# Performance work log

Measured on AMD Instinct MI355X. Metric: run time of the kernel, lower is better.

Reference implementation:

```python
import jax, jax.numpy as jnp
import numpy as np

D = 512  # common_dim

def _ln(x, g, b):
    m = jnp.mean(x, -1, keepdims=True)
    v = jnp.var(x, -1, keepdims=True)
    return g * (x - m) * jax.lax.rsqrt(v + 1e-5) + b

def _gelu(x):
    return jax.nn.gelu(x, approximate=False)  # torch nn.GELU default (erf)

def _mha(q, kv, Wi, bi, Wo, bo):
    # seq_len == 1: softmax over a single key is exactly 1 regardless of q/k,
    # so MultiheadAttention reduces to out_proj(v_proj(kv)); identical math,
    # and q/k projections receive exactly zero gradient either way.
    vp = kv @ Wi[:, 2 * D:] + bi[2 * D:]
    return vp @ Wo + bo

def setup_inputs() -> dict:
    key = jax.random.key(0)
    ks = iter(jax.random.split(key, 64))
    B, HID = 8192, 1024
    Fv, Fi, Ft = 10, 6, 15
    def rn(shape, s=0.02):
        return jax.random.normal(next(ks), shape, jnp.float32) * s
    return dict(
        verb_hidden=rn((B, HID), 1.0), verb_logits=rn((B, Fv), 1.0),
        inst_hidden=rn((B, HID), 1.0), inst_logits=rn((B, Fi), 1.0),
        target_hidden=rn((B, HID), 1.0), target_logits=rn((B, Ft), 1.0),
        # hidden_projection per task (order: verb, instrument, target)
        hp_W=rn((3, HID, D)), hp_b=jnp.zeros((3, D)), hp_g=jnp.ones((3, D)), hp_be=jnp.zeros((3, D)),
        # logit_projection per task (different in-dims)
        lp_W_verb=rn((Fv, D // 2)), lp_b_verb=jnp.zeros((D // 2,)),
        lp_W_inst=rn((Fi, D // 2)), lp_b_inst=jnp.zeros((D // 2,)),
        lp_W_target=rn((Ft, D // 2)), lp_b_target=jnp.zeros((D // 2,)),
        lp_g=jnp.ones((3, D // 2)), lp_be=jnp.zeros((3, D // 2)),
        # 4 MHA modules: [self, verb_inst, verb_target, inst_target]
        mha_in_W=rn((4, D, 3 * D)), mha_in_b=jnp.zeros((4, 3 * D)),
        mha_out_W=rn((4, D, D)), mha_out_b=jnp.zeros((4, D)),
        n1_g=jnp.ones((3, D)), n1_be=jnp.zeros((3, D)),
        n2_g=jnp.ones((3, D)), n2_be=jnp.zeros((3, D)),
        gate_W=rn((3, 2 * D, D)), gate_b=jnp.zeros((3, D)),
        fus_W1=rn((3 * D + 3 * (D // 2), D)), fus_b1=jnp.zeros((D,)),
        fus_g1=jnp.ones((D,)), fus_ge1=jnp.zeros((D,)),
        fus_W2=rn((D, D)), fus_b2=jnp.zeros((D,)),
        fus_g2=jnp.ones((D,)), fus_ge2=jnp.zeros((D,)),
    )

def reference(verb_hidden, verb_logits, inst_hidden, inst_logits, target_hidden, target_logits,
              hp_W, hp_b, hp_g, hp_be,
              lp_W_verb, lp_b_verb, lp_W_inst, lp_b_inst, lp_W_target, lp_b_target, lp_g, lp_be,
              mha_in_W, mha_in_b, mha_out_W, mha_out_b,
              n1_g, n1_be, n2_g, n2_be, gate_W, gate_b,
              fus_W1, fus_b1, fus_g1, fus_ge1, fus_W2, fus_b2, fus_g2, fus_ge2):
    # dropout is inference-mode identity
    def hproj(x, i):
        return _gelu(_ln(x @ hp_W[i] + hp_b[i], hp_g[i], hp_be[i]))
    def lproj(x, W, b, i):
        return _gelu(_ln(jax.nn.sigmoid(x) @ W + b, lp_g[i], lp_be[i]))

    verb_h, inst_h, target_h = hproj(verb_hidden, 0), hproj(inst_hidden, 1), hproj(target_hidden, 2)
    verb_l = lproj(verb_logits, lp_W_verb, lp_b_verb, 0)
    inst_l = lproj(inst_logits, lp_W_inst, lp_b_inst, 1)
    target_l = lproj(target_logits, lp_W_target, lp_b_target, 2)

    sa = lambda x: _mha(x, x, mha_in_W[0], mha_in_b[0], mha_out_W[0], mha_out_b[0])
    verb_e = _ln(verb_h + sa(verb_h), n1_g[0], n1_be[0])
    inst_e = _ln(inst_h + sa(inst_h), n1_g[1], n1_be[1])
    target_e = _ln(target_h + sa(target_h), n1_g[2], n1_be[2])

    ca = lambda i, q, kv: _mha(q, kv, mha_in_W[i], mha_in_b[i], mha_out_W[i], mha_out_b[i])
    v2i, i2v = ca(1, verb_e, inst_e), ca(1, inst_e, verb_e)
    v2t, t2v = ca(2, verb_e, target_e), ca(2, target_e, verb_e)
    i2t, t2i = ca(3, inst_e, target_e), ca(3, target_e, inst_e)

    def fuse(x, a, b, i):
        m = (a + b) * 0.5
        gate = jax.nn.sigmoid(jnp.concatenate([x, m], axis=1) @ gate_W[i] + gate_b[i])
        return _ln(x + gate * m, n2_g[i], n2_be[i])

    verb_f = fuse(verb_e, v2i, v2t, 0)
    inst_f = fuse(inst_e, i2v, i2t, 1)
    target_f = fuse(target_e, t2v, t2i, 2)

    comb = jnp.concatenate([verb_f, inst_f, target_f, verb_l, inst_l, target_l], axis=1)  # [B, 2304]
    h = _gelu(_ln(comb @ fus_W1 + fus_b1, fus_g1, fus_ge1))
    return _ln(h @ fus_W2 + fus_b2, fus_g2, fus_ge2)
```

## Files before the change

### kernel.cpp

```cpp
#include <hip/hip_runtime.h>
#include <math.h>

typedef unsigned short ushort_t;
using short8  = __attribute__((ext_vector_type(8))) short;
using floatx4 = __attribute__((ext_vector_type(4))) float;

__device__ __forceinline__ ushort_t f2bf(float f) {
  unsigned u = __builtin_bit_cast(unsigned, f);
  u = (u + 0x7fffu + ((u >> 16) & 1u)) >> 16;
  return (ushort_t)u;
}
__device__ __forceinline__ float bf2f(ushort_t u) {
  unsigned v = ((unsigned)u) << 16;
  return __builtin_bit_cast(float, v);
}

__device__ __forceinline__ void load_lds16(const ushort_t* g, ushort_t* l) {
  __builtin_amdgcn_global_load_lds(
      (const __attribute__((address_space(1))) unsigned int*)g,
      (__attribute__((address_space(3))) unsigned int*)l, 16, 0, 0);
}

struct Seg { const ushort_t* A; const ushort_t* W; int lda, ldw, K; };
struct GemmZ {
  ushort_t* Cb;
  ushort_t* CbT;
  const float* bias;
  float scale; int nseg; int mmax;
  Seg seg[6];
};
struct GemmArgs { GemmZ z[9]; };

template <int BM, int BK>
__device__ __forceinline__ void gemm_body(const GemmArgs& ga) {
  const GemmZ& gz = ga.z[blockIdx.z];
  if ((int)blockIdx.x >= gz.mmax) return;
  __shared__ ushort_t As[BM * BK];
  __shared__ ushort_t Bs[128 * BK];
  constexpr int TPR = BK / 8;
  constexpr int RPC = 2048 / BK;
  const int tid = threadIdx.x;
  const int wid = tid >> 6, lane = tid & 63, quad = lane >> 4, l16 = lane & 15;
  const int bm = blockIdx.x * BM, bn = blockIdx.y * 128;
  constexpr int MI = BM / 32;
  const int wm = (wid & 1) * (BM / 2), wn = (wid >> 1) * 64;
  floatx4 acc[MI][4] = {};
  const int srow = tid / TPR;
  const int scol = ((tid & (TPR - 1)) ^ (srow & (TPR - 1))) << 3;

  for (int s = 0; s < gz.nseg; s++) {
    const Seg sg = gz.seg[s];
    const ushort_t* aG = sg.A + (size_t)(bm + srow) * sg.lda + scol;
    const ushort_t* bG = sg.W + (size_t)(bn + srow) * sg.ldw + scol;
    for (int k0 = 0; k0 < sg.K; k0 += BK) {
      __syncthreads();
#pragma unroll
      for (int r = 0; r < BM / RPC; r++)
        load_lds16(aG + k0 + (size_t)(RPC * r) * sg.lda, As + r * 2048 + tid * 8);
#pragma unroll
      for (int r = 0; r < 128 / RPC; r++)
        load_lds16(bG + k0 + (size_t)(RPC * r) * sg.ldw, Bs + r * 2048 + tid * 8);
      __syncthreads();
#pragma unroll
      for (int sub = 0; sub < BK / 32; sub++) {
        const int sl = ((sub * 4 + quad) ^ (l16 & (TPR - 1))) << 3;
        short8 bw[4];
#pragma unroll
        for (int j = 0; j < 4; j++)
          bw[j] = *(const short8*)&Bs[(wn + 16 * j + l16) * BK + sl];
#pragma unroll
        for (int i = 0; i < MI; i++) {
          short8 af = *(const short8*)&As[(wm + 16 * i + l16) * BK + sl];
#pragma unroll
          for (int j = 0; j < 4; j++)
            acc[i][j] = __builtin_amdgcn_mfma_f32_16x16x32_bf16(af, bw[j], acc[i][j], 0, 0, 0);
        }
      }
    }
  }

#pragma unroll
  for (int i = 0; i < MI; i++) {
#pragma unroll
    for (int j = 0; j < 4; j++) {
      const int colg = bn + wn + 16 * j + l16;
      const float bb = gz.bias ? gz.bias[colg] : 0.f;
#pragma unroll
      for (int r = 0; r < 4; r++) {
        const int rowg = bm + wm + 16 * i + quad * 4 + r;
        const float v = (acc[i][j][r] + bb) * gz.scale;
        const ushort_t bo = f2bf(v);
        if (gz.Cb)  gz.Cb[(size_t)rowg * 512 + colg] = bo;
        if (gz.CbT) gz.CbT[(size_t)colg * 512 + rowg] = bo;
      }
    }
  }
}

__global__ __launch_bounds__(256) void gemm_L2(GemmArgs ga)  { gemm_body<128, 128>(ga); }
__global__ __launch_bounds__(256) void gemm_L4(GemmArgs ga)  { gemm_body<128, 128>(ga); }
__global__ __launch_bounds__(256) void gemm_L7(GemmArgs ga)  { gemm_body<128, 64>(ga); }
__global__ __launch_bounds__(256) void gemm_L9(GemmArgs ga)  { gemm_body<128, 64>(ga); }
__global__ __launch_bounds__(256) void gemm_L11(GemmArgs ga) { gemm_body<64, 128>(ga); }
__global__ __launch_bounds__(256) void gemm_L13(GemmArgs ga) { gemm_body<64, 128>(ga); }

__global__ __launch_bounds__(256) void row_ln(
    const ushort_t* __restrict__ P, const ushort_t* __restrict__ R,
    const ushort_t* __restrict__ cross,
    const float* __restrict__ gamma, const float* __restrict__ beta, int gstride,
    ushort_t* __restrict__ outb, float* __restrict__ outf, int mode, int gelu)
{
  const size_t S2 = (size_t)8192 * 512;
  const int wid = threadIdx.x >> 6, lane = threadIdx.x & 63;
  const int row = blockIdx.x * 4 + wid;
  const int t = row >> 13;
  const float* g  = gamma + t * gstride;
  const float* be = beta + t * gstride;
  const int c0 = lane * 8;
  const short8 pv = *(const short8*)&P[(size_t)row * 512 + c0];
  short8 rv = {}, av = {};
  if (mode >= 1) rv = *(const short8*)&R[(size_t)row * 512 + c0];
  if (mode == 2) av = *(const short8*)&cross[(size_t)t * S2 + (size_t)(row & 8191) * 512 + c0];
  float v[8], s = 0.f, ss = 0.f;
#pragma unroll
  for (int j = 0; j < 8; j++) {
    float x = bf2f((ushort_t)pv[j]);
    if (mode == 2) {
      const float sg = 1.f / (1.f + __expf(-x));
      x = bf2f((ushort_t)rv[j]) + sg * bf2f((ushort_t)av[j]);
    } else if (mode == 1) {
      x += bf2f((ushort_t)rv[j]);
    }
    v[j] = x; s += x; ss += x * x;
  }
#pragma unroll
  for (int off = 32; off > 0; off >>= 1) {
    s  += __shfl_xor(s,  off, 64);
    ss += __shfl_xor(ss, off, 64);
  }
  const float mean = s * (1.f / 512.f);
  const float var  = ss * (1.f / 512.f) - mean * mean;
  const float rstd = rsqrtf(var + 1e-5f);
  float gv[8], bv[8];
  *(float4*)&gv[0] = *(const float4*)&g[c0];
  *(float4*)&gv[4] = *(const float4*)&g[c0 + 4];
  *(float4*)&bv[0] = *(const float4*)&be[c0];
  *(float4*)&bv[4] = *(const float4*)&be[c0 + 4];
  float y[8];
#pragma unroll
  for (int j = 0; j < 8; j++) {
    float yy = gv[j] * ((v[j] - mean) * rstd) + bv[j];
    if (gelu) yy = 0.5f * yy * (1.f + erff(yy * 0.70710678118f));
    y[j] = yy;
  }
  if (outb) {
    short8 ov;
#pragma unroll
    for (int j = 0; j < 8; j++) ov[j] = (short)f2bf(y[j]);
    *(short8*)&outb[(size_t)row * 512 + c0] = ov;
  } else {
    *(float4*)&outf[(size_t)row * 512 + c0]     = *(float4*)&y[0];
    *(float4*)&outf[(size_t)row * 512 + c0 + 4] = *(float4*)&y[4];
  }
}

__global__ __launch_bounds__(256) void lproj3(
    const float* __restrict__ vl, const float* __restrict__ il, const float* __restrict__ tl,
    const float* __restrict__ Wv, const float* __restrict__ bv,
    const float* __restrict__ Wi, const float* __restrict__ bi,
    const float* __restrict__ Wt, const float* __restrict__ bt,
    const float* __restrict__ lp_g, const float* __restrict__ lp_be,
    ushort_t* __restrict__ out)
{
  const int set = blockIdx.y;
  const float* logits = set == 0 ? vl : set == 1 ? il : tl;
  const int F = set == 0 ? 10 : set == 1 ? 6 : 15;
  const float* W    = set == 0 ? Wv : set == 1 ? Wi : Wt;
  const float* bias = set == 0 ? bv : set == 1 ? bi : bt;
  const float* gamma = lp_g + set * 256;
  const float* beta  = lp_be + set * 256;
  ushort_t* o = out + (size_t)set * 8192 * 256;
  const int wid = threadIdx.x >> 6, lane = threadIdx.x & 63;
  const int row = blockIdx.x * 4 + wid;
  const int c0 = lane * 4;
  float sg[16];
  for (int f = 0; f < F; f++)
    sg[f] = 1.f / (1.f + __expf(-logits[(size_t)row * F + f]));
  float v[4], s = 0.f, ss = 0.f;
  *(float4*)&v[0] = *(const float4*)&bias[c0];
  for (int f = 0; f < F; f++) {
    const float4 w4 = *(const float4*)&W[f * 256 + c0];
#pragma unroll
    for (int j = 0; j < 4; j++) v[j] += sg[f] * w4[j];
  }
#pragma unroll
  for (int j = 0; j < 4; j++) { s += v[j]; ss += v[j] * v[j]; }
#pragma unroll
  for (int off = 32; off > 0; off >>= 1) {
    s  += __shfl_xor(s,  off, 64);
    ss += __shfl_xor(ss, off, 64);
  }
  const float mean = s * (1.f / 256.f);
  const float var  = ss * (1.f / 256.f) - mean * mean;
  const float rstd = rsqrtf(var + 1e-5f);
  const float4 g4 = *(const float4*)&gamma[c0];
  const float4 b4 = *(const float4*)&beta[c0];
  ushort4 ov;
  float y[4];
#pragma unroll
  for (int j = 0; j < 4; j++) {
    float yy = g4[j] * ((v[j] - mean) * rstd) + b4[j];
    yy = 0.5f * yy * (1.f + erff(yy * 0.70710678118f));
    y[j] = yy;
  }
  ov.x = f2bf(y[0]); ov.y = f2bf(y[1]); ov.z = f2bf(y[2]); ov.w = f2bf(y[3]);
  *(ushort4*)&o[(size_t)row * 256 + c0] = ov;
}

struct PrepArgs {
  const float *vh, *ih, *th;
  const float *mha_in_W, *mha_out_W, *mha_in_b, *mha_out_b;
  const float *hp_W, *gate_W, *fus_W1, *fus_W2;
  ushort_t *xbf, *Wvbf, *hpWt, *gateWt, *fusW1t, *fusW2t, *WoT;
  float *cb;
};

__global__ __launch_bounds__(256) void prep(PrepArgs pa) {
  __shared__ float tsh[32][33];
  const int b = blockIdx.x, tid = threadIdx.x;
  if (b < 24576) {
    const int mat = b >> 13, blk = b & 8191;
    const float* src = mat == 0 ? pa.vh : mat == 1 ? pa.ih : pa.th;
    const size_t i = (size_t)blk * 256 + tid;
    const float4 f = ((const float4*)src)[i];
    ushort4 o; o.x = f2bf(f.x); o.y = f2bf(f.y); o.z = f2bf(f.z); o.w = f2bf(f.w);
    ((ushort4*)(pa.xbf + (size_t)mat * 8192 * 1024))[i] = o;
    return;
  }
  if (b < 28672) {
    const int u = b - 24576, z = u >> 10, blk = u & 1023;
    const int idx = blk * 256 + tid, r = idx >> 9, c = idx & 511;
    pa.Wvbf[(size_t)z * 262144 + idx] =
        f2bf(pa.mha_in_W[(size_t)z * 786432 + (size_t)r * 1536 + 1024 + c]);
    return;
  }
  if (b >= 34176) {
    const int u2 = b - 34176;
    const int z = u2 >> 3, n0 = (u2 & 7) * 64;
    const int lane = tid & 63, wv = tid >> 6;
    const int o = lane & 15, p = lane >> 4;
    const int n = n0 + wv * 16 + o;
    const float* bv = pa.mha_in_b + z * 1536 + 1024;
    const float* Wo = pa.mha_out_W + (size_t)z * 262144;
    float a = 0.f;
#pragma unroll 4
    for (int kk = 0; kk < 128; kk++) {
      const int k = p * 128 + kk;
      a += bv[k] * Wo[(size_t)k * 512 + n];
    }
    a += __shfl_xor(a, 16, 64);
    a += __shfl_xor(a, 32, 64);
    if (p == 0) pa.cb[z * 512 + n] = a + pa.mha_out_b[z * 512 + n];
    return;
  }
  const float* tin; ushort_t* tout; int K, N, u; size_t izs, ozs;
  if (b < 30208)      { u = b - 28672; tin = pa.hp_W;      tout = pa.hpWt;   K = 1024; N = 512; izs = 524288; ozs = 524288; }
  else if (b < 31744) { u = b - 30208; tin = pa.gate_W;    tout = pa.gateWt; K = 1024; N = 512; izs = 524288; ozs = 524288; }
  else if (b < 32896) { u = b - 31744; tin = pa.fus_W1;    tout = pa.fusW1t; K = 2304; N = 512; izs = 0;      ozs = 0; }
  else if (b < 33152) { u = b - 32896; tin = pa.fus_W2;    tout = pa.fusW2t; K = 512;  N = 512; izs = 0;      ozs = 0; }
  else                { u = b - 33152; tin = pa.mha_out_W; tout = pa.WoT;    K = 512;  N = 512; izs = 262144; ozs = 262144; }
  const int nbx = N / 32, perz = nbx * (K / 32);
  const int z = u / perz, rem = u % perz, bx = rem % nbx, by = rem / nbx;
  tin += (size_t)z * izs; tout += (size_t)z * ozs;
  const int n0 = bx * 32, k0 = by * 32;
  const int tx = tid & 31, ty = tid >> 5;
#pragma unroll
  for (int r = 0; r < 32; r += 8)
    tsh[ty + r][tx] = tin[(size_t)(k0 + ty + r) * N + n0 + tx];
  __syncthreads();
#pragma unroll
  for (int r = 0; r < 32; r += 8)
    tout[(size_t)(n0 + ty + r) * K + k0 + tx] = f2bf(tsh[tx][ty + r]);
}

__global__ __launch_bounds__(256) void bias2_k(
    const float* __restrict__ cb, const float* __restrict__ gate_W,
    const float* __restrict__ gate_b, float* __restrict__ out,
    float* __restrict__ out2)
{
  const int t = blockIdx.z;
  const int m1[3] = {1, 1, 2}, m2[3] = {2, 3, 3};
  const float* c1 = cb + m1[t] * 512;
  const float* c2 = cb + m2[t] * 512;
  const float* W = gate_W + (size_t)t * 524288 + (size_t)512 * 512;
  const int tid = threadIdx.x;
  const int lane = tid & 63, wv = tid >> 6;
  const int o = lane & 15, p = lane >> 4;
  const int n = blockIdx.x * 64 + wv * 16 + o;
  float a = 0.f;
#pragma unroll 4
  for (int kk = 0; kk < 128; kk++) {
    const int k = p * 128 + kk;
    a += 0.5f * (c1[k] + c2[k]) * W[(size_t)k * 512 + n];
  }
  a += __shfl_xor(a, 16, 64);
  a += __shfl_xor(a, 32, 64);
  if (p == 0) {
    out[t * 512 + n] = a + gate_b[t * 512 + n];
    out2[t * 512 + n] = c1[n] + c2[n];
  }
}

extern "C" void kernel_launch(void* const* d_in, const int* in_sizes, int n_in,
                              void* d_out, int out_size, void* d_ws, size_t ws_size,
                              hipStream_t stream)
{
  const float* verb_hidden   = (const float*)d_in[0];
  const float* verb_logits   = (const float*)d_in[1];
  const float* inst_hidden   = (const float*)d_in[2];
  const float* inst_logits   = (const float*)d_in[3];
  const float* target_hidden = (const float*)d_in[4];
  const float* target_logits = (const float*)d_in[5];
  const float* hp_W  = (const float*)d_in[6];
  const float* hp_b  = (const float*)d_in[7];
  const float* hp_g  = (const float*)d_in[8];
  const float* hp_be = (const float*)d_in[9];
  const float* lp_W_verb   = (const float*)d_in[10];
  const float* lp_b_verb   = (const float*)d_in[11];
  const float* lp_W_inst   = (const float*)d_in[12];
  const float* lp_b_inst   = (const float*)d_in[13];
  const float* lp_W_target = (const float*)d_in[14];
  const float* lp_b_target = (const float*)d_in[15];
  const float* lp_g  = (const float*)d_in[16];
  const float* lp_be = (const float*)d_in[17];
  const float* mha_in_W  = (const float*)d_in[18];
  const float* mha_in_b  = (const float*)d_in[19];
  const float* mha_out_W = (const float*)d_in[20];
  const float* mha_out_b = (const float*)d_in[21];
  const float* n1_g  = (const float*)d_in[22];
  const float* n1_be = (const float*)d_in[23];
  const float* n2_g  = (const float*)d_in[24];
  const float* n2_be = (const float*)d_in[25];
  const float* gate_W = (const float*)d_in[26];
  const float* gate_b = (const float*)d_in[27];
  const float* fus_W1 = (const float*)d_in[28];
  const float* fus_b1 = (const float*)d_in[29];
  const float* fus_g1 = (const float*)d_in[30];
  const float* fus_ge1= (const float*)d_in[31];
  const float* fus_W2 = (const float*)d_in[32];
  const float* fus_b2 = (const float*)d_in[33];
  const float* fus_g2 = (const float*)d_in[34];
  const float* fus_ge2= (const float*)d_in[35];

  char* w = (char*)d_ws;
  const size_t S2 = (size_t)8192 * 512;
  const size_t MB = 1024 * 1024;
  ushort_t* xbf     = (ushort_t*)(w);
  ushort_t* crossbf = (ushort_t*)(w);
  ushort_t* gbf     = (ushort_t*)(w);
  ushort_t* Pbig    = (ushort_t*)(w + 48 * MB);
  ushort_t* hbf     = (ushort_t*)(w + 72 * MB);
  ushort_t* fbf     = (ushort_t*)(w + 72 * MB);
  ushort_t* ebf     = (ushort_t*)(w + 96 * MB);
  ushort_t* lbf     = (ushort_t*)(w + 120 * MB);
  char* wp = w + 132 * MB;
  ushort_t* hpWt    = (ushort_t*)(wp);
  ushort_t* gateWt  = (ushort_t*)(wp + 3145728);
  ushort_t* fusW1t  = (ushort_t*)(wp + 6291456);
  ushort_t* fusW2t  = (ushort_t*)(wp + 8650752);
  ushort_t* WoT     = (ushort_t*)(wp + 9175040);
  ushort_t* Wvbf    = (ushort_t*)(wp + 11272192);
  ushort_t* CWt     = (ushort_t*)(wp + 13369344);
  ushort_t* CWplain = (ushort_t*)(wp + 15466496);
  ushort_t* Gt      = (ushort_t*)(wp + 17563648);
  float*    cb      = (float*)(wp + 20709376);
  float*    bias2   = (float*)(wp + 20717568);
  float*    cbsum   = (float*)(wp + 20723712);

  dim3 blk(256);
  const int mods[3][2] = {{1, 2}, {1, 3}, {2, 3}};
  const int srcs[3][2] = {{1, 2}, {0, 2}, {0, 1}};

  {
    PrepArgs pa;
    pa.vh = verb_hidden; pa.ih = inst_hidden; pa.th = target_hidden;
    pa.mha_in_W = mha_in_W; pa.mha_out_W = mha_out_W;
    pa.mha_in_b = mha_in_b; pa.mha_out_b = mha_out_b;
    pa.hp_W = hp_W; pa.gate_W = gate_W; pa.fus_W1 = fus_W1; pa.fus_W2 = fus_W2;
    pa.xbf = xbf; pa.Wvbf = Wvbf; pa.hpWt = hpWt; pa.gateWt = gateWt;
    pa.fusW1t = fusW1t; pa.fusW2t = fusW2t; pa.WoT = WoT; pa.cb = cb;
    prep<<<34208, blk, 0, stream>>>(pa);
  }

  {
    GemmArgs ga{};
    for (int z = 0; z < 4; z++) {
      GemmZ& g = ga.z[z];
      g.Cb = CWplain + (size_t)z * 262144; g.CbT = CWt + (size_t)z * 262144;
      g.scale = 1.f; g.nseg = 1; g.mmax = 4;
      g.seg[0] = {Wvbf + (size_t)z * 262144, WoT + (size_t)z * 262144, 512, 512, 512};
    }
    gemm_L2<<<dim3(4, 4, 4), blk, 0, stream>>>(ga);
  }

  bias2_k<<<dim3(8, 1, 3), blk, 0, stream>>>(cb, gate_W, gate_b, bias2, cbsum);

  {
    GemmArgs ga{};
    for (int z = 0; z < 3; z++) {
      GemmZ& g = ga.z[z];
      g.Cb = Pbig + (size_t)z * S2; g.bias = hp_b + z * 512;
      g.scale = 1.f; g.nseg = 1; g.mmax = 64;
      g.seg[0] = {xbf + (size_t)z * 8192 * 1024, hpWt + (size_t)z * 524288, 1024, 1024, 1024};
    }
    for (int idx = 0; idx < 6; idx++) {
      const int t = idx >> 1, u = idx & 1, m = mods[t][u];
      GemmZ& g = ga.z[3 + idx];
      g.Cb = Gt + (size_t)idx * 262144; g.scale = 0.5f; g.nseg = 1; g.mmax = 4;
      g.seg[0] = {gateWt + (size_t)t * 524288 + 512, CWplain + (size_t)m * 262144, 1024, 512, 512};
    }
    gemm_L4<<<dim3(64, 4, 9), blk, 0, stream>>>(ga);
  }

  lproj3<<<dim3(2048, 3), blk, 0, stream>>>(verb_logits, inst_logits, target_logits,
      lp_W_verb, lp_b_verb, lp_W_inst, lp_b_inst, lp_W_target, lp_b_target,
      lp_g, lp_be, lbf);

  row_ln<<<6144, blk, 0, stream>>>(Pbig, nullptr, nullptr, hp_g, hp_be, 512,
                                   hbf, nullptr, 0, 1);

  {
    GemmArgs ga{};
    GemmZ& g = ga.z[0];
    g.Cb = Pbig; g.bias = cb; g.scale = 1.f; g.nseg = 1; g.mmax = 192;
    g.seg[0] = {hbf, CWt, 512, 512, 512};
    gemm_L7<<<dim3(192, 4, 1), blk, 0, stream>>>(ga);
  }
  row_ln<<<6144, blk, 0, stream>>>(Pbig, hbf, nullptr, n1_g, n1_be, 512,
                                   ebf, nullptr, 1, 0);

  {
    GemmArgs ga{};
    for (int t = 0; t < 3; t++) {
      GemmZ& g = ga.z[t];
      g.Cb = crossbf + (size_t)t * S2;
      g.bias = cbsum + t * 512; g.scale = 0.5f; g.nseg = 2; g.mmax = 64;
      g.seg[0] = {ebf + (size_t)srcs[t][0] * S2, CWt + (size_t)mods[t][0] * 262144, 512, 512, 512};
      g.seg[1] = {ebf + (size_t)srcs[t][1] * S2, CWt + (size_t)mods[t][1] * 262144, 512, 512, 512};
    }
    for (int t = 0; t < 3; t++) {
      GemmZ& g = ga.z[3 + t];
      g.Cb = Pbig + (size_t)t * S2; g.bias = bias2 + t * 512;
      g.scale = 1.f; g.nseg = 3; g.mmax = 64;
      g.seg[0] = {ebf + (size_t)t * S2,           gateWt + (size_t)t * 524288, 512, 1024, 512};
      g.seg[1] = {ebf + (size_t)srcs[t][0] * S2,  Gt + (size_t)(2 * t) * 262144,     512, 512, 512};
      g.seg[2] = {ebf + (size_t)srcs[t][1] * S2,  Gt + (size_t)(2 * t + 1) * 262144, 512, 512, 512};
    }
    gemm_L9<<<dim3(64, 4, 6), blk, 0, stream>>>(ga);
  }

  row_ln<<<6144, blk, 0, stream>>>(Pbig, ebf, crossbf, n2_g, n2_be, 512,
                                   fbf, nullptr, 2, 0);

  {
    GemmArgs ga{};
    GemmZ& g = ga.z[0];
    g.Cb = Pbig; g.bias = fus_b1; g.scale = 1.f; g.nseg = 6; g.mmax = 128;
    g.seg[0] = {fbf,                          fusW1t,        512, 2304, 512};
    g.seg[1] = {fbf + S2,                     fusW1t + 512,  512, 2304, 512};
    g.seg[2] = {fbf + 2 * S2,                 fusW1t + 1024, 512, 2304, 512};
    g.seg[3] = {lbf,                          fusW1t + 1536, 256, 2304, 256};
    g.seg[4] = {lbf + (size_t)8192 * 256,     fusW1t + 1792, 256, 2304, 256};
    g.seg[5] = {lbf + (size_t)2 * 8192 * 256, fusW1t + 2048, 256, 2304, 256};
    gemm_L11<<<dim3(128, 4, 1), blk, 0, stream>>>(ga);
  }
  row_ln<<<2048, blk, 0, stream>>>(Pbig, nullptr, nullptr, fus_g1, fus_ge1, 0,
                                   gbf, nullptr, 0, 1);
  {
    GemmArgs ga{};
    GemmZ& g = ga.z[0];
    g.Cb = Pbig; g.bias = fus_b2; g.scale = 1.f; g.nseg = 1; g.mmax = 128;
    g.seg[0] = {gbf, fusW2t, 512, 512, 512};
    gemm_L13<<<dim3(128, 4, 1), blk, 0, stream>>>(ga);
  }
  row_ln<<<2048, blk, 0, stream>>>(Pbig, nullptr, nullptr, fus_g2, fus_ge2, 0,
                                   nullptr, (float*)d_out, 0, 0);
}
```

Baseline: 544.4 us.

## Fuse cross-attention and gate GEMMs sharing A tiles with sigmoid-gating epilogue

Replaces the six-slice grouped GEMM (three cross-attention sums and three gate pre-activations) with one kernel per task. Each A tile of the shared activations is loaded once and multiplied against both the cross weights and the gate weights. The epilogue applies the bias, the 0.5 mean and the sigmoid gate directly, so only gate*m is written. This removes a second read of the activations, one intermediate output buffer, and the extra cross read in the following layernorm. The cost is more accumulator registers (two 4x4 tile sets) and more LDS per block, which may lower occupancy.

```diff
diff --git a/kernel.cpp b/kernel.cpp
--- a/kernel.cpp
+++ b/kernel.cpp
@@ -100,9 +100,115 @@
 __global__ __launch_bounds__(256) void gemm_L2(GemmArgs ga)  { gemm_body<128, 128>(ga); }
 __global__ __launch_bounds__(256) void gemm_L4(GemmArgs ga)  { gemm_body<128, 128>(ga); }
 __global__ __launch_bounds__(256) void gemm_L7(GemmArgs ga)  { gemm_body<128, 64>(ga); }
-__global__ __launch_bounds__(256) void gemm_L9(GemmArgs ga)  { gemm_body<128, 64>(ga); }
 __global__ __launch_bounds__(256) void gemm_L11(GemmArgs ga) { gemm_body<64, 128>(ga); }
 __global__ __launch_bounds__(256) void gemm_L13(GemmArgs ga) { gemm_body<64, 128>(ga); }
+
+struct L9fArgs {
+  const ushort_t *ebf, *CWt, *gateWt, *Gt;
+  const float *cbsum, *bias2;
+  ushort_t *out;
+};
+
+__global__ __launch_bounds__(256) void gemm_L9f(L9fArgs pa) {
+  const int t = blockIdx.z;
+  const int mA[3] = {1, 1, 2}, mB[3] = {2, 3, 3};
+  const int sA[3] = {1, 0, 0}, sB[3] = {2, 2, 1};
+  const size_t S2 = (size_t)8192 * 512;
+  __shared__ ushort_t As[128 * 64];
+  __shared__ ushort_t Bm[128 * 64];
+  __shared__ ushort_t Bg[128 * 64];
+  const int tid = threadIdx.x;
+  const int wid = tid >> 6, lane = tid & 63, quad = lane >> 4, l16 = lane & 15;
+  const int bm = blockIdx.x * 128, bn = blockIdx.y * 128;
+  const int wm = (wid & 1) * 64, wn = (wid >> 1) * 64;
+  floatx4 am[4][4] = {}, ag[4][4] = {};
+  const int srow = tid >> 3;
+  const int scol = ((tid & 7) ^ (srow & 7)) << 3;
+  const int x7 = l16 & 7;
+
+  {
+    const ushort_t* aG = pa.ebf + (size_t)t * S2 + (size_t)(bm + srow) * 512 + scol;
+    const ushort_t* gG = pa.gateWt + (size_t)t * 524288 + (size_t)(bn + srow) * 1024 + scol;
+    for (int k0 = 0; k0 < 512; k0 += 64) {
+      __syncthreads();
+#pragma unroll
+      for (int r = 0; r < 4; r++) {
+        load_lds16(aG + k0 + (size_t)(32 * r) * 512,  As + r * 2048 + tid * 8);
+        load_lds16(gG + k0 + (size_t)(32 * r) * 1024, Bg + r * 2048 + tid * 8);
+      }
+      __syncthreads();
+#pragma unroll
+      for (int sub = 0; sub < 2; sub++) {
+        const int sl = ((sub * 4 + quad) ^ x7) << 3;
+        short8 bg_[4];
+#pragma unroll
+        for (int j = 0; j < 4; j++)
+          bg_[j] = *(const short8*)&Bg[(wn + 16 * j + l16) * 64 + sl];
+#pragma unroll
+        for (int i = 0; i < 4; i++) {
+          const short8 af = *(const short8*)&As[(wm + 16 * i + l16) * 64 + sl];
+#pragma unroll
+          for (int j = 0; j < 4; j++)
+            ag[i][j] = __builtin_amdgcn_mfma_f32_16x16x32_bf16(af, bg_[j], ag[i][j], 0, 0, 0);
+        }
+      }
+    }
+  }
+  for (int s = 1; s < 3; s++) {
+    const int src = (s == 1) ? sA[t] : sB[t];
+    const int mod = (s == 1) ? mA[t] : mB[t];
+    const ushort_t* aG = pa.ebf + (size_t)src * S2 + (size_t)(bm + srow) * 512 + scol;
+    const ushort_t* mG = pa.CWt + (size_t)mod * 262144 + (size_t)(bn + srow) * 512 + scol;
+    const ushort_t* gG = pa.Gt + (size_t)(2 * t + s - 1) * 262144 + (size_t)(bn + srow) * 512 + scol;
+    for (int k0 = 0; k0 < 512; k0 += 64) {
+      __syncthreads();
+#pragma unroll
+      for (int r = 0; r < 4; r++) {
+        load_lds16(aG + k0 + (size_t)(32 * r) * 512, As + r * 2048 + tid * 8);
+        load_lds16(mG + k0 + (size_t)(32 * r) * 512, Bm + r * 2048 + tid * 8);
+        load_lds16(gG + k0 + (size_t)(32 * r) * 512, Bg + r * 2048 + tid * 8);
+      }
+      __syncthreads();
+#pragma unroll
+      for (int sub = 0; sub < 2; sub++) {
+        const int sl = ((sub * 4 + quad) ^ x7) << 3;
+        short8 bm_[4], bg_[4];
+#pragma unroll
+        for (int j = 0; j < 4; j++) {
+          bm_[j] = *(const short8*)&Bm[(wn + 16 * j + l16) * 64 + sl];
+          bg_[j] = *(const short8*)&Bg[(wn + 16 * j + l16) * 64 + sl];
+        }
+#pragma unroll
+        for (int i = 0; i < 4; i++) {
+          const short8 af = *(const short8*)&As[(wm + 16 * i + l16) * 64 + sl];
+#pragma unroll
+          for (int j = 0; j < 4; j++) {
+            am[i][j] = __builtin_amdgcn_mfma_f32_16x16x32_bf16(af, bm_[j], am[i][j], 0, 0, 0);
+            ag[i][j] = __builtin_amdgcn_mfma_f32_16x16x32_bf16(af, bg_[j], ag[i][j], 0, 0, 0);
+          }
+        }
+      }
+    }
+  }
+
+#pragma unroll
+  for (int i = 0; i < 4; i++) {
+#pragma unroll
+    for (int j = 0; j < 4; j++) {
+      const int colg = bn + wn + 16 * j + l16;
+      const float cbs = pa.cbsum[t * 512 + colg];
+      const float b2  = pa.bias2[t * 512 + colg];
+#pragma unroll
+      for (int r = 0; r < 4; r++) {
+        const int rowg = bm + wm + 16 * i + quad * 4 + r;
+        const float msum = (am[i][j][r] + cbs) * 0.5f;
+        const float gpre = ag[i][j][r] + b2;
+        const float rr = msum / (1.f + __expf(-gpre));
+        pa.out[(size_t)t * S2 + (size_t)rowg * 512 + colg] = f2bf(rr);
+      }
+    }
+  }
+}
 
 __global__ __launch_bounds__(256) void row_ln(
     const ushort_t* __restrict__ P, const ushort_t* __restrict__ R,
@@ -379,7 +485,6 @@
 
   dim3 blk(256);
   const int mods[3][2] = {{1, 2}, {1, 3}, {2, 3}};
-  const int srcs[3][2] = {{1, 2}, {0, 2}, {0, 1}};
 
   {
     PrepArgs pa;
@@ -440,27 +545,14 @@
                                    ebf, nullptr, 1, 0);
 
   {
-    GemmArgs ga{};
-    for (int t = 0; t < 3; t++) {
-      GemmZ& g = ga.z[t];
-      g.Cb = crossbf + (size_t)t * S2;
-      g.bias = cbsum + t * 512; g.scale = 0.5f; g.nseg = 2; g.mmax = 64;
-      g.seg[0] = {ebf + (size_t)srcs[t][0] * S2, CWt + (size_t)mods[t][0] * 262144, 512, 512, 512};
-      g.seg[1] = {ebf + (size_t)srcs[t][1] * S2, CWt + (size_t)mods[t][1] * 262144, 512, 512, 512};
-    }
-    for (int t = 0; t < 3; t++) {
-      GemmZ& g = ga.z[3 + t];
-      g.Cb = Pbig + (size_t)t * S2; g.bias = bias2 + t * 512;
-      g.scale = 1.f; g.nseg = 3; g.mmax = 64;
-      g.seg[0] = {ebf + (size_t)t * S2,           gateWt + (size_t)t * 524288, 512, 1024, 512};
-      g.seg[1] = {ebf + (size_t)srcs[t][0] * S2,  Gt + (size_t)(2 * t) * 262144,     512, 512, 512};
-      g.seg[2] = {ebf + (size_t)srcs[t][1] * S2,  Gt + (size_t)(2 * t + 1) * 262144, 512, 512, 512};
-    }
-    gemm_L9<<<dim3(64, 4, 6), blk, 0, stream>>>(ga);
-  }
-
-  row_ln<<<6144, blk, 0, stream>>>(Pbig, ebf, crossbf, n2_g, n2_be, 512,
-                                   fbf, nullptr, 2, 0);
+    L9fArgs pa;
+    pa.ebf = ebf; pa.CWt = CWt; pa.gateWt = gateWt; pa.Gt = Gt;
+    pa.cbsum = cbsum; pa.bias2 = bias2; pa.out = crossbf;
+    gemm_L9f<<<dim3(64, 4, 3), blk, 0, stream>>>(pa);
+  }
+
+  row_ln<<<6144, blk, 0, stream>>>(crossbf, ebf, nullptr, n2_g, n2_be, 512,
+                                   fbf, nullptr, 1, 0);
 
   {
     GemmArgs ga{};
```

Measured after the change: 562.2 us. 1.03x slower.
